# Performance work log

Hardware: AMD Instinct MI355X
Metric: run time of the kernel (lower is better)

## Reference

```python
import jax, jax.numpy as jnp
import numpy as np

NUM_ITEMS = 50000
EMBED_DIM = 100
HIDDEN_DIM = 200
BATCH = 1024
SEQ_LEN = 200


def setup_inputs() -> dict:
    key = jax.random.key(0)
    ks = jax.random.split(key, 8)
    q = jax.random.randint(ks[0], (BATCH, SEQ_LEN), 0, NUM_ITEMS, dtype=jnp.int32)
    embed = jax.random.normal(ks[1], (NUM_ITEMS, EMBED_DIM), jnp.float32) * 0.05
    # GRU weights, concatenated along gate axis in order (r, z, n)
    Wi = jax.random.normal(ks[2], (EMBED_DIM, 3 * HIDDEN_DIM), jnp.float32) * (1.0 / np.sqrt(EMBED_DIM))
    bi = jnp.zeros((3 * HIDDEN_DIM,), jnp.float32)  # input-side biases (flax dense_i has bias)
    Wh = jax.random.normal(ks[3], (HIDDEN_DIM, 3 * HIDDEN_DIM), jnp.float32) * (1.0 / np.sqrt(HIDDEN_DIM))
    bhn = jnp.zeros((HIDDEN_DIM,), jnp.float32)  # only the 'hn' hidden dense has a bias in flax GRUCell
    Wo = jax.random.normal(ks[4], (HIDDEN_DIM, NUM_ITEMS), jnp.float32) * (1.0 / np.sqrt(HIDDEN_DIM))
    bo = jnp.zeros((NUM_ITEMS,), jnp.float32)
    return {"q": q, "embed": embed, "Wi": Wi, "bi": bi, "Wh": Wh, "bhn": bhn, "Wo": Wo, "bo": bo}


def reference(q, embed, Wi, bi, Wh, bhn, Wo, bo):
    # mask padding id 0, then embed
    not_zero = (q != 0).astype(jnp.float32)[..., None]        # [B,T,1]
    x = jnp.take(embed, q, axis=0) * not_zero                 # [B,T,E]
    H = Wh.shape[0]

    def step(h, xt):
        gi = xt @ Wi + bi                                     # [B,3H]
        gh = h @ Wh                                           # [B,3H]
        ir, iz, inn = jnp.split(gi, 3, axis=-1)
        hr, hz, hn = jnp.split(gh, 3, axis=-1)
        r = jax.nn.sigmoid(ir + hr)
        z = jax.nn.sigmoid(iz + hz)
        n = jnp.tanh(inn + r * (hn + bhn))
        h_new = (1.0 - z) * n + z * h                          # flax GRUCell update
        return h_new, None

    h0 = jnp.zeros((q.shape[0], H), jnp.float32)
    xT = jnp.swapaxes(x, 0, 1)                                # [T,B,E]
    h_last, _ = jax.lax.scan(step, h0, xT)
    return h_last @ Wo + bo                                    # [B, num_items]
```

## Files before the change

### kernel.cpp

```cpp
#include <hip/hip_runtime.h>

#define BATCH 1024
#define TT    200
#define EE    100
#define HH    200
#define GG    600
#define NI    50000
#define NKT   7
#define KPAD  224
#define HSTR  264
#define NTILE3 3125
#define NTW   50
#define KTW   4

typedef _Float16 half8 __attribute__((ext_vector_type(8)));
typedef _Float16 half4v __attribute__((ext_vector_type(4)));
typedef float   float4v __attribute__((ext_vector_type(4)));

static __device__ __forceinline__ float4v mfma16(half8 a, half8 b, float4v c) {
    return __builtin_amdgcn_mfma_f32_16x16x32_f16(a, b, c, 0, 0, 0);
}

#if __has_builtin(__builtin_amdgcn_rcpf)
static __device__ __forceinline__ float fastrcp(float x) { return __builtin_amdgcn_rcpf(x); }
#else
static __device__ __forceinline__ float fastrcp(float x) { return 1.f / x; }
#endif

static __device__ __forceinline__ float sigm(float x) {
    return fastrcp(1.f + __expf(-x));
}
static __device__ __forceinline__ float tanh_fast(float x) {
    float e = __expf(2.f * fabsf(x));
    float t = 1.f - 2.f * fastrcp(e + 1.f);
    return __builtin_copysignf(t, x);
}

__global__ __launch_bounds__(64) void repack_all(const float* __restrict__ Wi,
                                                 const float* __restrict__ bi,
                                                 const float* __restrict__ Wh,
                                                 half8* __restrict__ Wif,
                                                 float* __restrict__ biP,
                                                 half8* __restrict__ Whf) {
    const int bx   = blockIdx.x;
    const int lane = threadIdx.x;
    const int l15  = lane & 15;
    const int lhi  = lane >> 4;
    if (bx < NTW * KTW) {
        const int kt = bx & 3;
        const int nt = bx >> 2;
        const int np = nt * 16 + l15;
        const int c  = np >> 2;
        const int g  = np & 3;
        half8 v;
        #pragma unroll
        for (int j = 0; j < 8; ++j) {
            int k = kt * 32 + lhi * 8 + j;
            float w = (k < EE && g < 3) ? Wi[(size_t)k * GG + g * HH + c] : 0.f;
            v[j] = (_Float16)w;
        }
        Wif[(size_t)bx * 64 + lane] = v;
        if (kt == 0 && lhi == 0)
            biP[np] = (g < 3) ? bi[g * HH + c] : 0.f;
    } else {
        const int b2   = bx - NTW * KTW;
        const int kt   = b2 % NKT;
        const int tile = b2 / NKT;
        const int g    = tile / 16;
        const int tc   = tile % 16;
        const int col  = tc * 16 + l15;
        half8 v;
        #pragma unroll
        for (int j = 0; j < 8; ++j) {
            int k = kt * 32 + lhi * 8 + j;
            float w = (k < HH && col < HH) ? Wh[(size_t)k * GG + g * HH + col] : 0.f;
            v[j] = (_Float16)w;
        }
        Whf[(size_t)b2 * 64 + lane] = v;
    }
}

__global__ __launch_bounds__(256) void ewi_mfma(const float* __restrict__ embed,
                                                const half8* __restrict__ Wif,
                                                const float* __restrict__ biP,
                                                _Float16* __restrict__ EWi16) {
    const int tid  = threadIdx.x;
    const int w    = tid >> 6;
    const int lane = tid & 63;
    const int l15  = lane & 15;
    const int lhi  = lane >> 4;

    const int mtb   = (blockIdx.x * 4 + w) * 2;
    const bool liveA = (mtb < NTILE3);
    const bool liveB = (mtb + 1 < NTILE3);
    if (!liveA) return;
    const int i0a = mtb * 16;
    const int i0b = liveB ? (mtb + 1) * 16 : i0a;

    half8 aA[KTW], aB[KTW];
    #pragma unroll
    for (int kt = 0; kt < KTW; ++kt) {
        const int k0 = kt * 32 + lhi * 8;
        const float* erA = embed + (size_t)(i0a + l15) * EE + k0;
        const float* erB = embed + (size_t)(i0b + l15) * EE + k0;
        #pragma unroll
        for (int j = 0; j < 8; ++j) {
            aA[kt][j] = (k0 + j < EE) ? (_Float16)erA[j] : (_Float16)0.f;
            aB[kt][j] = (k0 + j < EE) ? (_Float16)erB[j] : (_Float16)0.f;
        }
    }

    for (int nt = 0; nt < NTW; ++nt) {
        const half8* bfp = Wif + (size_t)nt * KTW * 64 + lane;
        float4v accA = (float4v){0.f, 0.f, 0.f, 0.f};
        float4v accB = (float4v){0.f, 0.f, 0.f, 0.f};
        #pragma unroll
        for (int kt = 0; kt < KTW; ++kt) {
            const half8 bf = bfp[kt * 64];
            accA = mfma16(aA[kt], bf, accA);
            accB = mfma16(aB[kt], bf, accB);
        }
        const float biv = biP[nt * 16 + l15];
        #pragma unroll
        for (int r = 0; r < 4; ++r) {
            const int rowA = i0a + lhi * 4 + r;
            float valA = accA[r] + biv;
            if (rowA == 0) valA = biv;
            EWi16[(size_t)rowA * 800 + nt * 16 + l15] = (_Float16)valA;
        }
        if (liveB) {
            #pragma unroll
            for (int r = 0; r < 4; ++r) {
                const int rowB = i0b + lhi * 4 + r;
                EWi16[(size_t)rowB * 800 + nt * 16 + l15] = (_Float16)(accB[r] + biv);
            }
        }
    }
}

__global__ __launch_bounds__(256, 1) void scan_mfma(const int* __restrict__ q,
                                                    const _Float16* __restrict__ EWi16,
                                                    const half8* __restrict__ Whf,
                                                    const float* __restrict__ bhn,
                                                    _Float16* __restrict__ h16g) {
    __shared__ __align__(16) _Float16 hbuf[2][16 * HSTR];
    __shared__ __align__(16) float accbuf[39 * 64];
    __shared__ int qs[4][TT];

    const int tid  = threadIdx.x;
    const int w    = tid >> 6;
    const int lane = tid & 63;
    const int l15  = lane & 15;
    const int lhi  = lane >> 4;
    const int b0   = blockIdx.x * 4;

    for (int idx = tid; idx < 2 * 16 * HSTR; idx += 256)
        ((_Float16*)hbuf)[idx] = (_Float16)0.f;
    for (int idx = tid; idx < 4 * TT; idx += 256) {
        int b = idx / TT, t = idx % TT;
        qs[b][t] = q[(size_t)(b0 + b) * TT + t];
    }

    half8 wb[10][NKT];
    #pragma unroll
    for (int i = 0; i < 10; ++i) {
        int tau = w + 4 * i;
        if (tau > 38) tau = 38;
        const int g  = (tau >= 26) ? 2 : (tau >= 13 ? 1 : 0);
        const int tc = tau - g * 13;
        #pragma unroll
        for (int kt = 0; kt < NKT; ++kt)
            wb[i][kt] = Whf[((size_t)(g * 16 + tc) * NKT + kt) * 64 + lane];
    }
    const bool has9 = (w < 3);

    const int cb = lane & 3;
    const int cc = (lane >> 2) & 15;
    float bhn_s[4]; bool creal[4]; int cga[4];
    #pragma unroll
    for (int j = 0; j < 4; ++j) {
        const int tc = j * 4 + w;
        const int cg = tc * 16 + cc;
        creal[j] = (tc < 13) && (cg < HH);
        cga[j]   = cg;
        bhn_s[j] = creal[j] ? bhn[cg] : 0.f;
    }
    float hreg[4] = {0.f, 0.f, 0.f, 0.f};

    __syncthreads();

    half4v gA[4], gB[4];
    #define LOADGI(G, tt) do {                                               \
        const int tl = (tt) < TT ? (tt) : (TT - 1);                          \
        const int qv = qs[cb][tl];                                           \
        const _Float16* ew = EWi16 + (size_t)qv * 800;                       \
        G[0] = *(const half4v*)(ew + (size_t)(w * 16 + cc) * 4);             \
        G[1] = *(const half4v*)(ew + (size_t)((4 + w) * 16 + cc) * 4);       \
        G[2] = *(const half4v*)(ew + (size_t)((8 + w) * 16 + cc) * 4);       \
        if (w == 0 && creal[3])                                              \
            G[3] = *(const half4v*)(ew + (size_t)(192 + cc) * 4);            \
    } while (0)

    LOADGI(gA, 0);
    LOADGI(gB, 1);

    #define STEP(CUR, NXT, G, TLOAD) do {                                    \
        const _Float16* hb = &hbuf[CUR][0];                                  \
        float4v acc[10];                                                     \
        _Pragma("unroll")                                                    \
        for (int i = 0; i < 10; ++i) acc[i] = (float4v){0.f, 0.f, 0.f, 0.f}; \
        _Pragma("unroll")                                                    \
        for (int kt = 0; kt < NKT; ++kt) {                                   \
            const half8 af = *(const half8*)(hb + l15 * HSTR + kt * 32 + lhi * 8); \
            _Pragma("unroll")                                                \
            for (int i = 0; i < 9; ++i)                                      \
                acc[i] = mfma16(af, wb[i][kt], acc[i]);                      \
            if (has9) acc[9] = mfma16(af, wb[9][kt], acc[9]);                \
        }                                                                    \
                  \
        if (lane < 16) {                                                     \
            _Pragma("unroll")                                                \
            for (int i = 0; i < 9; ++i)                                      \
                *(float4v*)&accbuf[(w + 4 * i) * 64 + l15 * 4] = acc[i];     \
            if (has9) *(float4v*)&accbuf[(w + 36) * 64 + l15 * 4] = acc[9];  \
        }                                                                    \
        __syncthreads();                      \
        _Float16* hn = &hbuf[NXT][0];                                        \
        _Pragma("unroll")                                                    \
        for (int j = 0; j < 4; ++j) {                                        \
            const int tc = j * 4 + w;                                        \
            if (tc < 13) {                                 \
                const float aR = accbuf[(0 * 13 + tc) * 64 + lane];          \
                const float aZ = accbuf[(1 * 13 + tc) * 64 + lane];          \
                const float aN = accbuf[(2 * 13 + tc) * 64 + lane];          \
                if (creal[j]) {                                              \
                    float rr = sigm((float)G[j][0] + aR);                    \
                    float zz = sigm((float)G[j][1] + aZ);                    \
                    float nn = tanh_fast((float)G[j][2] + rr * (aN + bhn_s[j])); \
                    float hv = (1.f - zz) * nn + zz * hreg[j];               \
                    hreg[j] = hv;                                            \
                    hn[cb * HSTR + cga[j]] = (_Float16)hv;                   \
                }                                                            \
            }                                                                \
        }                                                                    \
        LOADGI(G, TLOAD);     \
        __syncthreads();                                        \
    } while (0)

    for (int t = 0; t < TT; t += 2) {
        STEP(0, 1, gA, t + 2);
        STEP(1, 0, gB, t + 3);
    }
    #undef STEP
    #undef LOADGI

    for (int idx = tid; idx < 4 * KPAD; idx += 256) {
        int b = idx / KPAD, k = idx % KPAD;
        h16g[(size_t)(b0 + b) * KPAD + k] = hbuf[0][b * HSTR + k];
    }
}

__global__ __launch_bounds__(256) void out_mfma(const _Float16* __restrict__ h16g,
                                                const float* __restrict__ Wo,
                                                const float* __restrict__ bo,
                                                float* __restrict__ out) {
    const int tid  = threadIdx.x;
    const int w    = tid >> 6;
    const int lane = tid & 63;
    const int l15  = lane & 15;
    const int lhi  = lane >> 4;

    const int ntb   = (blockIdx.x * 4 + w) * 2;
    const bool liveA = (ntb < NTILE3);
    const bool liveB = (ntb + 1 < NTILE3);
    const int ntA = liveA ? ntb : (NTILE3 - 1);
    const int ntB = liveB ? (ntb + 1) : (NTILE3 - 1);
    const int colA = ntA * 16 + l15;
    const int colB = ntB * 16 + l15;

    half8 wbA[7], wbB[7];
    #pragma unroll
    for (int kt = 0; kt < NKT; ++kt) {
        #pragma unroll
        for (int j = 0; j < 8; ++j) {
            int k = kt * 32 + lhi * 8 + j;
            wbA[kt][j] = (k < HH) ? (_Float16)Wo[(size_t)k * NI + colA] : (_Float16)0.f;
            wbB[kt][j] = (k < HH) ? (_Float16)Wo[(size_t)k * NI + colB] : (_Float16)0.f;
        }
    }
    const float bovA = bo[colA];
    const float bovB = bo[colB];

    for (int mt = 0; mt < BATCH / 16; ++mt) {
        const _Float16* hrow = h16g + (size_t)(mt * 16 + l15) * KPAD + lhi * 8;
        float4v accA = (float4v){0.f, 0.f, 0.f, 0.f};
        float4v accB = (float4v){0.f, 0.f, 0.f, 0.f};
        #pragma unroll
        for (int kt = 0; kt < NKT; ++kt) {
            const half8 af = *(const half8*)(hrow + kt * 32);
            accA = mfma16(af, wbA[kt], accA);
            accB = mfma16(af, wbB[kt], accB);
        }
        if (liveA) {
            #pragma unroll
            for (int r = 0; r < 4; ++r) {
                int row = mt * 16 + lhi * 4 + r;
                out[(size_t)row * NI + colA] = accA[r] + bovA;
            }
        }
        if (liveB) {
            #pragma unroll
            for (int r = 0; r < 4; ++r) {
                int row = mt * 16 + lhi * 4 + r;
                out[(size_t)row * NI + colB] = accB[r] + bovB;
            }
        }
    }
}

extern "C" void kernel_launch(void* const* d_in, const int* in_sizes, int n_in,
                              void* d_out, int out_size, void* d_ws, size_t ws_size,
                              hipStream_t stream) {
    const int*   q     = (const int*)d_in[0];
    const float* embed = (const float*)d_in[1];
    const float* Wi    = (const float*)d_in[2];
    const float* bi    = (const float*)d_in[3];
    const float* Wh    = (const float*)d_in[4];
    const float* bhn   = (const float*)d_in[5];
    const float* Wo    = (const float*)d_in[6];
    const float* bo    = (const float*)d_in[7];
    float* out = (float*)d_out;

    _Float16* EWi16 = (_Float16*)d_out;
    half8*    Whf   = (half8*)((char*)d_out + 120000000);
    half8*    Wif   = (half8*)((char*)d_out + 121000000);
    float*    biP   = (float*)((char*)d_out + 122000000);
    _Float16* h16g  = (_Float16*)d_ws;

    repack_all<<<NTW * KTW + 48 * NKT, 64, 0, stream>>>(Wi, bi, Wh, Wif, biP, Whf);
    ewi_mfma<<<(NTILE3 / 2 + 3) / 4, 256, 0, stream>>>(embed, Wif, biP, EWi16);
    scan_mfma<<<BATCH / 4, 256, 0, stream>>>(q, EWi16, Whf, bhn, h16g);
    out_mfma<<<(NTILE3 / 2 + 3) / 4 + 1, 256, 0, stream>>>(h16g, Wo, bo, out);
}
```

Baseline: 463.5 us.

## Split GRU scan across 12 waves and fold hn bias into recurrent weights

The recurrent scan kernel now runs 768 threads (12 waves) per block instead of 256. Each wave holds 4 of the 39 gate tiles of Wh in registers instead of 10, and each thread updates one hidden element (plus a second for the tail) instead of four. The hn bias is folded into Wh as an extra K row, fed by a constant 1.0 column in the hidden-state buffer, which removes the per-step bias add. The gate-input prefetch depth drops from two steps to one. The aim is to shorten the per-step serial critical path through more parallelism and lower register pressure, at the cost of larger barriers and a shorter prefetch lead.

New measurement: 403.1 us. -13.0%, faster.

```diff
diff --git a/kernel.cpp b/kernel.cpp
--- a/kernel.cpp
+++ b/kernel.cpp
@@ -39,6 +39,7 @@
 __global__ __launch_bounds__(64) void repack_all(const float* __restrict__ Wi,
                                                  const float* __restrict__ bi,
                                                  const float* __restrict__ Wh,
+                                                 const float* __restrict__ bhn,
                                                  half8* __restrict__ Wif,
                                                  float* __restrict__ biP,
                                                  half8* __restrict__ Whf) {
@@ -73,7 +74,11 @@
         #pragma unroll
         for (int j = 0; j < 8; ++j) {
             int k = kt * 32 + lhi * 8 + j;
-            float w = (k < HH && col < HH) ? Wh[(size_t)k * GG + g * HH + col] : 0.f;
+            float w = 0.f;
+            if (col < HH) {
+                if (k < HH)                      w = Wh[(size_t)k * GG + g * HH + col];
+                else if (g == 2 && k == HH)      w = bhn[col];
+            }
             v[j] = (_Float16)w;
         }
         Whf[(size_t)b2 * 64 + lane] = v;
@@ -138,10 +143,9 @@
     }
 }
 
-__global__ __launch_bounds__(256, 1) void scan_mfma(const int* __restrict__ q,
+__global__ __launch_bounds__(768, 3) void scan_mfma(const int* __restrict__ q,
                                                     const _Float16* __restrict__ EWi16,
                                                     const half8* __restrict__ Whf,
-                                                    const float* __restrict__ bhn,
                                                     _Float16* __restrict__ h16g) {
     __shared__ __align__(16) _Float16 hbuf[2][16 * HSTR];
     __shared__ __align__(16) float accbuf[39 * 64];
@@ -154,17 +158,18 @@
     const int lhi  = lane >> 4;
     const int b0   = blockIdx.x * 4;
 
-    for (int idx = tid; idx < 2 * 16 * HSTR; idx += 256)
-        ((_Float16*)hbuf)[idx] = (_Float16)0.f;
-    for (int idx = tid; idx < 4 * TT; idx += 256) {
+    for (int idx = tid; idx < 2 * 16 * HSTR; idx += 768)
+        ((_Float16*)hbuf)[idx] = (idx % HSTR == HH) ? (_Float16)1.0f : (_Float16)0.f;
+    for (int idx = tid; idx < 4 * TT; idx += 768) {
         int b = idx / TT, t = idx % TT;
         qs[b][t] = q[(size_t)(b0 + b) * TT + t];
     }
 
-    half8 wb[10][NKT];
+    const bool s3 = (w < 3);
+    half8 wb[4][NKT];
     #pragma unroll
-    for (int i = 0; i < 10; ++i) {
-        int tau = w + 4 * i;
+    for (int i = 0; i < 4; ++i) {
+        int tau = w + 12 * i;
         if (tau > 38) tau = 38;
         const int g  = (tau >= 26) ? 2 : (tau >= 13 ? 1 : 0);
         const int tc = tau - g * 13;
@@ -172,89 +177,83 @@
         for (int kt = 0; kt < NKT; ++kt)
             wb[i][kt] = Whf[((size_t)(g * 16 + tc) * NKT + kt) * 64 + lane];
     }
-    const bool has9 = (w < 3);
-
-    const int cb = lane & 3;
-    const int cc = (lane >> 2) & 15;
-    float bhn_s[4]; bool creal[4]; int cga[4];
-    #pragma unroll
-    for (int j = 0; j < 4; ++j) {
-        const int tc = j * 4 + w;
-        const int cg = tc * 16 + cc;
-        creal[j] = (tc < 13) && (cg < HH);
-        cga[j]   = cg;
-        bhn_s[j] = creal[j] ? bhn[cg] : 0.f;
-    }
-    float hreg[4] = {0.f, 0.f, 0.f, 0.f};
+
+    const int cb    = tid & 3;
+    const int ccol  = tid >> 2;
+    const bool has2 = (tid < 32);
+    const int ccol2 = 192 + (tid >> 2);
+
+    float hreg = 0.f, hreg2 = 0.f;
 
     __syncthreads();
 
-    half4v gA[4], gB[4];
-    #define LOADGI(G, tt) do {                                               \
+    half4v G, G2;
+    #define LOADGI(tt) do {                                                  \
         const int tl = (tt) < TT ? (tt) : (TT - 1);                          \
         const int qv = qs[cb][tl];                                           \
         const _Float16* ew = EWi16 + (size_t)qv * 800;                       \
-        G[0] = *(const half4v*)(ew + (size_t)(w * 16 + cc) * 4);             \
-        G[1] = *(const half4v*)(ew + (size_t)((4 + w) * 16 + cc) * 4);       \
-        G[2] = *(const half4v*)(ew + (size_t)((8 + w) * 16 + cc) * 4);       \
-        if (w == 0 && creal[3])                                              \
-            G[3] = *(const half4v*)(ew + (size_t)(192 + cc) * 4);            \
+        G = *(const half4v*)(ew + ccol * 4);                                 \
+        if (has2) G2 = *(const half4v*)(ew + ccol2 * 4);                     \
     } while (0)
 
-    LOADGI(gA, 0);
-    LOADGI(gB, 1);
-
-    #define STEP(CUR, NXT, G, TLOAD) do {                                    \
+    LOADGI(0);
+
+    #define STEP(CUR, NXT, TLOAD) do {                                       \
         const _Float16* hb = &hbuf[CUR][0];                                  \
-        float4v acc[10];                                                     \
+        float4v acc[4];                                                      \
         _Pragma("unroll")                                                    \
-        for (int i = 0; i < 10; ++i) acc[i] = (float4v){0.f, 0.f, 0.f, 0.f}; \
+        for (int i = 0; i < 4; ++i) acc[i] = (float4v){0.f, 0.f, 0.f, 0.f};  \
         _Pragma("unroll")                                                    \
         for (int kt = 0; kt < NKT; ++kt) {                                   \
             const half8 af = *(const half8*)(hb + l15 * HSTR + kt * 32 + lhi * 8); \
             _Pragma("unroll")                                                \
-            for (int i = 0; i < 9; ++i)                                      \
+            for (int i = 0; i < 3; ++i)                                      \
                 acc[i] = mfma16(af, wb[i][kt], acc[i]);                      \
-            if (has9) acc[9] = mfma16(af, wb[9][kt], acc[9]);                \
+            if (s3) acc[3] = mfma16(af, wb[3][kt], acc[3]);                  \
         }                                                                    \
-                  \
+               \
         if (lane < 16) {                                                     \
             _Pragma("unroll")                                                \
-            for (int i = 0; i < 9; ++i)                                      \
-                *(float4v*)&accbuf[(w + 4 * i) * 64 + l15 * 4] = acc[i];     \
-            if (has9) *(float4v*)&accbuf[(w + 36) * 64 + l15 * 4] = acc[9];  \
+            for (int i = 0; i < 3; ++i)                                      \
+                *(float4v*)&accbuf[(w + 12 * i) * 64 + l15 * 4] = acc[i];    \
+            if (s3) *(float4v*)&accbuf[(w + 36) * 64 + l15 * 4] = acc[3];    \
         }                                                                    \
-        __syncthreads();                      \
+        __syncthreads();                               \
         _Float16* hn = &hbuf[NXT][0];                                        \
-        _Pragma("unroll")                                                    \
-        for (int j = 0; j < 4; ++j) {                                        \
-            const int tc = j * 4 + w;                                        \
-            if (tc < 13) {                                 \
-                const float aR = accbuf[(0 * 13 + tc) * 64 + lane];          \
-                const float aZ = accbuf[(1 * 13 + tc) * 64 + lane];          \
-                const float aN = accbuf[(2 * 13 + tc) * 64 + lane];          \
-                if (creal[j]) {                                              \
-                    float rr = sigm((float)G[j][0] + aR);                    \
-                    float zz = sigm((float)G[j][1] + aZ);                    \
-                    float nn = tanh_fast((float)G[j][2] + rr * (aN + bhn_s[j])); \
-                    float hv = (1.f - zz) * nn + zz * hreg[j];               \
-                    hreg[j] = hv;                                            \
-                    hn[cb * HSTR + cga[j]] = (_Float16)hv;                   \
-                }                                                            \
-            }                                                                \
+        {                                                                    \
+            const float aR = accbuf[tid];                                    \
+            const float aZ = accbuf[832 + tid];                              \
+            const float aN = accbuf[1664 + tid];                             \
+            float rr = sigm((float)G[0] + aR);                               \
+            float zz = sigm((float)G[1] + aZ);                               \
+            float nn = tanh_fast((float)G[2] + rr * aN);                     \
+            float hv = (1.f - zz) * nn + zz * hreg;                          \
+            hreg = hv;                                                       \
+            hn[cb * HSTR + ccol] = (_Float16)hv;                             \
         }                                                                    \
-        LOADGI(G, TLOAD);     \
-        __syncthreads();                                        \
+        if (has2) {                                                          \
+            const float aR = accbuf[768 + tid];                              \
+            const float aZ = accbuf[1600 + tid];                             \
+            const float aN = accbuf[2432 + tid];                             \
+            float rr = sigm((float)G2[0] + aR);                              \
+            float zz = sigm((float)G2[1] + aZ);                              \
+            float nn = tanh_fast((float)G2[2] + rr * aN);                    \
+            float hv = (1.f - zz) * nn + zz * hreg2;                         \
+            hreg2 = hv;                                                      \
+            hn[cb * HSTR + ccol2] = (_Float16)hv;                            \
+        }                                                                    \
+        LOADGI(TLOAD);        \
+        __syncthreads();             \
     } while (0)
 
     for (int t = 0; t < TT; t += 2) {
-        STEP(0, 1, gA, t + 2);
-        STEP(1, 0, gB, t + 3);
+        STEP(0, 1, t + 1);
+        STEP(1, 0, t + 2);
     }
     #undef STEP
     #undef LOADGI
 
-    for (int idx = tid; idx < 4 * KPAD; idx += 256) {
+    for (int idx = tid; idx < 4 * KPAD; idx += 768) {
         int b = idx / KPAD, k = idx % KPAD;
         h16g[(size_t)(b0 + b) * KPAD + k] = hbuf[0][b * HSTR + k];
     }
@@ -337,8 +336,8 @@
     float*    biP   = (float*)((char*)d_out + 122000000);
     _Float16* h16g  = (_Float16*)d_ws;
 
-    repack_all<<<NTW * KTW + 48 * NKT, 64, 0, stream>>>(Wi, bi, Wh, Wif, biP, Whf);
+    repack_all<<<NTW * KTW + 48 * NKT, 64, 0, stream>>>(Wi, bi, Wh, bhn, Wif, biP, Whf);
     ewi_mfma<<<(NTILE3 / 2 + 3) / 4, 256, 0, stream>>>(embed, Wif, biP, EWi16);
-    scan_mfma<<<BATCH / 4, 256, 0, stream>>>(q, EWi16, Whf, bhn, h16g);
+    scan_mfma<<<BATCH / 4, 768, 0, stream>>>(q, EWi16, Whf, h16g);
     out_mfma<<<(NTILE3 / 2 + 3) / 4 + 1, 256, 0, stream>>>(h16g, Wo, bo, out);
 }
```
